# Kernel tuning notes

Measured on AMD Instinct MI355X. Metric: run time of the kernel, lower is better.

## Reference

```python
import jax, jax.numpy as jnp
import numpy as np
from jax.scipy.special import logsumexp

B, T, S, F = 16, 4096, 32, 64
LOG2PI = float(np.log(2.0 * np.pi))


def setup_inputs() -> dict:
    key = jax.random.key(0)
    k1, k2, k3, k4, k5 = jax.random.split(key, 5)
    x = jax.random.normal(k1, (B, T, F), dtype=jnp.float32)
    means = jax.random.normal(k2, (S, F), dtype=jnp.float32)
    # PSD full covariance per state: A A^T + I  (MultivariateNormal covariance_matrix)
    A = 0.1 * jax.random.normal(k3, (S, F, F), dtype=jnp.float32)
    covs = jnp.einsum('sfg,shg->sfh', A, A) + jnp.eye(F, dtype=jnp.float32)
    # Row-stochastic transition matrix and initial distribution, in log space.
    log_A = jax.nn.log_softmax(jax.random.normal(k4, (S, S), dtype=jnp.float32), axis=-1)
    log_pi = jax.nn.log_softmax(jax.random.normal(k5, (S,), dtype=jnp.float32))
    mask = jnp.ones((B, T), dtype=bool)
    return {'x': x, 'means': means, 'covs': covs, 'log_A': log_A, 'log_pi': log_pi, 'mask': mask}


def _emission_logprob(x, means, covs):
    # Multivariate Gaussian log pdf per (batch, time, state): logB[b,t,s]
    Fdim = x.shape[-1]
    P = jnp.linalg.inv(covs)                       # [S,F,F] precision
    logdet = jnp.linalg.slogdet(covs)[1]           # [S]
    diff = x[:, :, None, :] - means[None, None]    # [B,T,S,F]
    maha = jnp.einsum('btsf,sfg,btsg->bts', diff, P, diff)
    return -0.5 * (maha + Fdim * LOG2PI + logdet)


def _fb_single(logB, mask, log_A, log_pi):
    # Forward-backward DP for one sequence. logB: [T,S], mask: [T].
    neg_inf = jnp.array(-jnp.inf, logB.dtype)

    def fstep(a_prev, inp):
        lb, m = inp
        a = logsumexp(a_prev[:, None] + log_A, axis=0) + lb  # alpha[t,j]
        a = jnp.where(m, a, neg_inf)
        return a, a

    a0 = jnp.where(mask[0], log_pi + logB[0], neg_inf)
    _, alphas = jax.lax.scan(fstep, a0, (logB[1:], mask[1:]))
    alpha = jnp.concatenate([a0[None], alphas], axis=0)      # [T,S]

    def bstep(b_next, inp):
        lb_next, m_next = inp
        b = logsumexp(log_A + (lb_next + b_next)[None, :], axis=1)  # beta[t,j]
        b = jnp.where(m_next, b, b_next)  # freeze at 0 past the last valid frame
        return b, b

    bT = jnp.zeros(logB.shape[1], dtype=logB.dtype)
    _, betas = jax.lax.scan(bstep, bT, (logB[1:], mask[1:]), reverse=True)
    beta = jnp.concatenate([betas, bT[None]], axis=0)        # [T,S]
    beta = jnp.where(mask[:, None], beta, neg_inf)
    return alpha, beta


def reference(x, means, covs, log_A, log_pi, mask):
    logB = _emission_logprob(x, means, covs)                  # [B,T,S]
    alpha, beta = jax.vmap(_fb_single, in_axes=(0, 0, None, None))(logB, mask, log_A, log_pi)
    lengths = mask.sum(axis=-1)                               # [B]
    idx = jnp.broadcast_to((lengths - 1)[:, None, None], (alpha.shape[0], 1, alpha.shape[2]))
    alpha_last = jnp.take_along_axis(alpha, idx, axis=1)[:, 0, :]
    evidence = logsumexp(alpha_last, axis=-1)                 # [B] log p(x_{1:l})
    gamma = alpha + beta - evidence[:, None, None]            # log posterior state marginals
    return gamma
```

## Files before the change

kernel.cpp:

```cpp
#include <hip/hip_runtime.h>
#include <math.h>

#define Tt 4096
#define NB 16

#define CLN2PI 1.8378770664093453f

#define OFF_W    0
#define OFF_D    131072
#define OFF_CST  133120
#define OFF_EV   133152
#define OFF_LB   133184
#define OFF_BET  2230336

__device__ __forceinline__ float rdlane(float x, int l) {
  return __int_as_float(__builtin_amdgcn_readlane(__float_as_int(x), l));
}

typedef unsigned int u32x2 __attribute__((ext_vector_type(2)));
__device__ __forceinline__ void xhalf(float v, float& lo, float& hi) {
  u32x2 r = __builtin_amdgcn_permlane32_swap(__float_as_uint(v), __float_as_uint(v),
                                             false, false);
  lo = __uint_as_float(r.x);
  hi = __uint_as_float(r.y);
}

__global__ __launch_bounds__(64) void k_chol(const float* __restrict__ covs,
                                             const float* __restrict__ means,
                                             float* __restrict__ ws) {
  __shared__ float Am[64][65];
  __shared__ float Wl[64][65];
  int s = blockIdx.x, j = threadIdx.x;
  for (int r = 0; r < 64; ++r) {
    Am[r][j] = covs[((size_t)s * 64 + r) * 64 + j];
    Wl[r][j] = 0.f;
  }
  __syncthreads();
  for (int k = 0; k < 64; ++k) {
    float diag = sqrtf(Am[k][k]);
    float col = (j > k) ? Am[j][k] / diag : 0.f;
    __syncthreads();
    if (j == k) Am[k][k] = diag;
    if (j > k)  Am[j][k] = col;
    __syncthreads();
    if (j > k) {
      for (int g = k + 1; g <= j; ++g) Am[j][g] -= col * Am[g][k];
    }
    __syncthreads();
  }
  {
    int c = j;
    Wl[c][c] = 1.0f / Am[c][c];
    for (int f = c + 1; f < 64; ++f) {
      float ssum = 0.f;
      for (int g = c; g < f; ++g) ssum += Am[f][g] * Wl[g][c];
      Wl[f][c] = -ssum / Am[f][f];
    }
  }
  __syncthreads();
  for (int r = 0; r < 64; ++r)
    ws[OFF_W + ((size_t)s * 64 + r) * 64 + j] = Wl[r][j];
  {
    float acc = 0.f;
    for (int g = 0; g < 64; ++g) acc += Wl[j][g] * means[s * 64 + g];
    ws[OFF_D + s * 64 + j] = acc;
  }
  if (j == 0) {
    float logdet = 0.f;
    for (int k = 0; k < 64; ++k) logdet += __logf(Am[k][k]);
    logdet *= 2.0f;
    ws[OFF_CST + s] = 64.0f * CLN2PI + logdet;
  }
}

__global__ __launch_bounds__(64) void k_emis(const float* __restrict__ x,
                                             const float* __restrict__ wsr,
                                             float* __restrict__ lb) {
  const float* W = wsr + OFF_W;
  const float* D = wsr + OFF_D;
  const float* C = wsr + OFF_CST;
  int bx = blockIdx.x;
  int sgrp = bx & 3;
  int pt = (bx >> 2) * 64 + threadIdx.x;
  const float* xr = x + (size_t)pt * 64;
  float xv[64];
#pragma unroll
  for (int c = 0; c < 16; ++c) {
    float4 q = ((const float4*)xr)[c];
    xv[4 * c + 0] = q.x; xv[4 * c + 1] = q.y;
    xv[4 * c + 2] = q.z; xv[4 * c + 3] = q.w;
  }
#pragma unroll 1
  for (int si = 0; si < 8; ++si) {
    int s = sgrp * 8 + si;
    const float* Ws = W + (size_t)s * 4096;
    const float* Ds = D + s * 64;
    float maha = 0.f;
#pragma unroll
    for (int f = 0; f < 64; ++f) {
      float z = -Ds[f];
#pragma unroll
      for (int ch = 0; ch < 4; ++ch) {
        if (ch <= (f >> 4)) {
#pragma unroll
          for (int gg = 0; gg < 16; ++gg) {
            int g = ch * 16 + gg;
            z = fmaf(Ws[f * 64 + g], xv[g], z);
          }
        }
      }
      maha = fmaf(z, z, maha);
    }
    lb[(size_t)pt * 32 + s] = -0.5f * (maha + C[s]);
  }
}

__device__ __forceinline__ float npsum32(const float* z) {
  float r[8];
#pragma unroll
  for (int k = 0; k < 8; ++k)
    r[k] = ((z[k] + z[k + 8]) + z[k + 16]) + z[k + 24];
  return ((r[0] + r[1]) + (r[2] + r[3])) + ((r[4] + r[5]) + (r[6] + r[7]));
}
__device__ __forceinline__ float max32(const float* z) {
  float t16[16];
#pragma unroll
  for (int k = 0; k < 16; ++k) t16[k] = fmaxf(z[k], z[k + 16]);
  float t8[8];
#pragma unroll
  for (int k = 0; k < 8; ++k) t8[k] = fmaxf(t16[k], t16[k + 8]);
  float t4[4];
#pragma unroll
  for (int k = 0; k < 4; ++k) t4[k] = fmaxf(t8[k], t8[k + 4]);
  float t2a = fmaxf(t4[0], t4[2]), t2b = fmaxf(t4[1], t4[3]);
  return fmaxf(t2a, t2b);
}
__device__ __forceinline__ float max16(const float* z) {
  float t8[8];
#pragma unroll
  for (int k = 0; k < 8; ++k) t8[k] = fmaxf(z[k], z[k + 8]);
  float t4[4];
#pragma unroll
  for (int k = 0; k < 4; ++k) t4[k] = fmaxf(t8[k], t8[k + 4]);
  return fmaxf(fmaxf(t4[0], t4[2]), fmaxf(t4[1], t4[3]));
}
__device__ __forceinline__ float sum16(const float* e) {
  float t8[8];
#pragma unroll
  for (int k = 0; k < 8; ++k) t8[k] = e[k] + e[k + 8];
  float t4[4];
#pragma unroll
  for (int k = 0; k < 4; ++k) t4[k] = t8[k] + t8[k + 4];
  return (t4[0] + t4[2]) + (t4[1] + t4[3]);
}

__global__ __launch_bounds__(64, 1) __attribute__((amdgpu_waves_per_eu(1)))
void k_fb(const float* __restrict__ logA,
          const float* __restrict__ logpi,
          float* __restrict__ ws,
          float* __restrict__ out) {
  const float* lbg = ws + OFF_LB;
  float* bet = ws + OFF_BET;
  float* ev  = ws + OFF_EV;
  int chain = blockIdx.x;
  int b   = chain & 15;
  int dir = chain >> 4;
  int lane = threadIdx.x;
  int j = lane & 31;
  int h = lane >> 5;
  int i0 = h << 4;
  const float* lb = lbg + (size_t)b * Tt * 32;

  if (dir == 0) {
    float acol[16];
#pragma unroll
    for (int k = 0; k < 16; ++k) {
      acol[k] = logA[(i0 + k) * 32 + j];
      asm volatile("" : "+v"(acol[k]));
    }
    float* ao = out + (size_t)b * Tt * 32;
    float a = logpi[j] + lb[j];
    ao[j] = a;
    float bA = lb[32 + j];
    float bB = lb[64 + j];
    float bC = lb[96 + j];
#pragma unroll 1
    for (int t = 1; t < Tt; ++t) {
      float bcur = bA; bA = bB; bB = bC;
      if (t + 3 < Tt) bC = lb[(size_t)(t + 3) * 32 + j];
      float sa[32];
#pragma unroll
      for (int i = 0; i < 32; ++i) sa[i] = rdlane(a, i);
      float z[16];
      if (h == 0) {
#pragma unroll
        for (int k = 0; k < 16; ++k) z[k] = sa[k] + acol[k];
      } else {
#pragma unroll
        for (int k = 0; k < 16; ++k) z[k] = sa[16 + k] + acol[k];
      }
      float mh = max16(z);
      float mlo, mhi;
      xhalf(mh, mlo, mhi);
      float m = fmaxf(mlo, mhi);
      float e[16];
#pragma unroll
      for (int k = 0; k < 16; ++k) e[k] = __expf(z[k] - m);
      float sh = sum16(e);
      float slo, shi;
      xhalf(sh, slo, shi);
      float S = slo + shi;
      a = (__logf(S) + m) + bcur;
      ao[(size_t)t * 32 + j] = a;
    }
    float z[32];
#pragma unroll
    for (int i = 0; i < 32; ++i) z[i] = rdlane(a, i);
    float m = max32(z);
#pragma unroll
    for (int i = 0; i < 32; ++i) z[i] = __expf(z[i] - m);
    float S = npsum32(z);
    if (lane == 0) ev[b] = __logf(S) + m;
  } else {
    float arow[16];
#pragma unroll
    for (int k = 0; k < 16; ++k) {
      arow[k] = logA[j * 32 + i0 + k];
      asm volatile("" : "+v"(arow[k]));
    }
    float* bo = bet + (size_t)b * Tt * 32;
    bo[(size_t)(Tt - 1) * 32 + j] = 0.f;
    float y = lb[(size_t)(Tt - 1) * 32 + j] + 0.f;
    float bA = lb[(size_t)(Tt - 2) * 32 + j];
    float bB = lb[(size_t)(Tt - 3) * 32 + j];
    float bC = lb[(size_t)(Tt - 4) * 32 + j];
#pragma unroll 1
    for (int t = Tt - 2; t >= 0; --t) {
      float bcur = bA; bA = bB; bB = bC;
      if (t >= 3) bC = lb[(size_t)(t - 3) * 32 + j];
      float sy[32];
#pragma unroll
      for (int i = 0; i < 32; ++i) sy[i] = rdlane(y, i);
      float z[16];
      if (h == 0) {
#pragma unroll
        for (int k = 0; k < 16; ++k) z[k] = arow[k] + sy[k];
      } else {
#pragma unroll
        for (int k = 0; k < 16; ++k) z[k] = arow[k] + sy[16 + k];
      }
      float mh = max16(z);
      float mlo, mhi;
      xhalf(mh, mlo, mhi);
      float m = fmaxf(mlo, mhi);
      float e[16];
#pragma unroll
      for (int k = 0; k < 16; ++k) e[k] = __expf(z[k] - m);
      float sh = sum16(e);
      float slo, shi;
      xhalf(sh, slo, shi);
      float S = slo + shi;
      float bv = __logf(S) + m;
      bo[(size_t)t * 32 + j] = bv;
      y = bcur + bv;
    }
  }
}

__global__ void k_gamma(const float* __restrict__ ws, float* __restrict__ out) {
  size_t idx = (size_t)blockIdx.x * blockDim.x + threadIdx.x;
  if (idx >= (size_t)NB * Tt * 32) return;
  int b = (int)(idx >> 17);
  float a  = out[idx];
  float bb = ws[OFF_BET + idx];
  float e  = ws[OFF_EV + b];
  out[idx] = (a + bb) - e;
}

extern "C" void kernel_launch(void* const* d_in, const int* in_sizes, int n_in,
                              void* d_out, int out_size, void* d_ws, size_t ws_size,
                              hipStream_t stream) {
  const float* x     = (const float*)d_in[0];
  const float* means = (const float*)d_in[1];
  const float* covs  = (const float*)d_in[2];
  const float* logA  = (const float*)d_in[3];
  const float* logpi = (const float*)d_in[4];
  float* ws  = (float*)d_ws;
  float* out = (float*)d_out;

  k_chol<<<dim3(32), dim3(64), 0, stream>>>(covs, means, ws);
  k_emis<<<dim3(4096), dim3(64), 0, stream>>>(x, ws, ws + OFF_LB);
  k_fb<<<dim3(32), dim3(64), 0, stream>>>(logA, logpi, ws, out);
  k_gamma<<<dim3(8192), dim3(256), 0, stream>>>(ws, out);
}
```

Measured before the change: 2.221 ms.

## Interleave forward and backward recursions in one wave per sequence

Instead of running the forward and backward chains in separate single-wave blocks (32 blocks), each block now runs both chains for one sequence in the same loop iteration (16 blocks). The two chains are independent, so interleaving them gives the scheduler instruction-level parallelism to hide the long dependent readlane/exp/log latency of each step. The cost is higher register pressure and twice the per-iteration work in one wave, which may not beat running the chains as separate waves on separate CUs.

```diff
diff --git a/kernel.cpp b/kernel.cpp
--- a/kernel.cpp
+++ b/kernel.cpp
@@ -162,109 +162,107 @@
   const float* lbg = ws + OFF_LB;
   float* bet = ws + OFF_BET;
   float* ev  = ws + OFF_EV;
-  int chain = blockIdx.x;
-  int b   = chain & 15;
-  int dir = chain >> 4;
+  int b   = blockIdx.x;
   int lane = threadIdx.x;
   int j = lane & 31;
   int h = lane >> 5;
   int i0 = h << 4;
   const float* lb = lbg + (size_t)b * Tt * 32;
-
-  if (dir == 0) {
-    float acol[16];
-#pragma unroll
-    for (int k = 0; k < 16; ++k) {
-      acol[k] = logA[(i0 + k) * 32 + j];
-      asm volatile("" : "+v"(acol[k]));
-    }
-    float* ao = out + (size_t)b * Tt * 32;
-    float a = logpi[j] + lb[j];
-    ao[j] = a;
-    float bA = lb[32 + j];
-    float bB = lb[64 + j];
-    float bC = lb[96 + j];
+  float* ao = out + (size_t)b * Tt * 32;
+  float* bo = bet + (size_t)b * Tt * 32;
+
+  float acol[16];
+  float arow[16];
+#pragma unroll
+  for (int k = 0; k < 16; ++k) {
+    acol[k] = logA[(i0 + k) * 32 + j];
+    asm volatile("" : "+v"(acol[k]));
+  }
+#pragma unroll
+  for (int k = 0; k < 16; ++k) {
+    arow[k] = logA[j * 32 + i0 + k];
+    asm volatile("" : "+v"(arow[k]));
+  }
+
+  float aF = logpi[j] + lb[j];
+  ao[j] = aF;
+  float fA = lb[32 + j];
+  float fB = lb[64 + j];
+  float fC = lb[96 + j];
+  bo[(size_t)(Tt - 1) * 32 + j] = 0.f;
+  float yB = lb[(size_t)(Tt - 1) * 32 + j] + 0.f;
+  float gA = lb[(size_t)(Tt - 2) * 32 + j];
+  float gB = lb[(size_t)(Tt - 3) * 32 + j];
+  float gC = lb[(size_t)(Tt - 4) * 32 + j];
+
 #pragma unroll 1
-    for (int t = 1; t < Tt; ++t) {
-      float bcur = bA; bA = bB; bB = bC;
-      if (t + 3 < Tt) bC = lb[(size_t)(t + 3) * 32 + j];
-      float sa[32];
-#pragma unroll
-      for (int i = 0; i < 32; ++i) sa[i] = rdlane(a, i);
-      float z[16];
-      if (h == 0) {
-#pragma unroll
-        for (int k = 0; k < 16; ++k) z[k] = sa[k] + acol[k];
-      } else {
-#pragma unroll
-        for (int k = 0; k < 16; ++k) z[k] = sa[16 + k] + acol[k];
-      }
-      float mh = max16(z);
-      float mlo, mhi;
-      xhalf(mh, mlo, mhi);
-      float m = fmaxf(mlo, mhi);
-      float e[16];
-#pragma unroll
-      for (int k = 0; k < 16; ++k) e[k] = __expf(z[k] - m);
-      float sh = sum16(e);
-      float slo, shi;
-      xhalf(sh, slo, shi);
-      float S = slo + shi;
-      a = (__logf(S) + m) + bcur;
-      ao[(size_t)t * 32 + j] = a;
-    }
-    float z[32];
-#pragma unroll
-    for (int i = 0; i < 32; ++i) z[i] = rdlane(a, i);
-    float m = max32(z);
-#pragma unroll
-    for (int i = 0; i < 32; ++i) z[i] = __expf(z[i] - m);
-    float S = npsum32(z);
-    if (lane == 0) ev[b] = __logf(S) + m;
-  } else {
-    float arow[16];
-#pragma unroll
-    for (int k = 0; k < 16; ++k) {
-      arow[k] = logA[j * 32 + i0 + k];
-      asm volatile("" : "+v"(arow[k]));
-    }
-    float* bo = bet + (size_t)b * Tt * 32;
-    bo[(size_t)(Tt - 1) * 32 + j] = 0.f;
-    float y = lb[(size_t)(Tt - 1) * 32 + j] + 0.f;
-    float bA = lb[(size_t)(Tt - 2) * 32 + j];
-    float bB = lb[(size_t)(Tt - 3) * 32 + j];
-    float bC = lb[(size_t)(Tt - 4) * 32 + j];
-#pragma unroll 1
-    for (int t = Tt - 2; t >= 0; --t) {
-      float bcur = bA; bA = bB; bB = bC;
-      if (t >= 3) bC = lb[(size_t)(t - 3) * 32 + j];
-      float sy[32];
-#pragma unroll
-      for (int i = 0; i < 32; ++i) sy[i] = rdlane(y, i);
-      float z[16];
-      if (h == 0) {
-#pragma unroll
-        for (int k = 0; k < 16; ++k) z[k] = arow[k] + sy[k];
-      } else {
-#pragma unroll
-        for (int k = 0; k < 16; ++k) z[k] = arow[k] + sy[16 + k];
-      }
-      float mh = max16(z);
-      float mlo, mhi;
-      xhalf(mh, mlo, mhi);
-      float m = fmaxf(mlo, mhi);
-      float e[16];
-#pragma unroll
-      for (int k = 0; k < 16; ++k) e[k] = __expf(z[k] - m);
-      float sh = sum16(e);
-      float slo, shi;
-      xhalf(sh, slo, shi);
-      float S = slo + shi;
-      float bv = __logf(S) + m;
-      bo[(size_t)t * 32 + j] = bv;
-      y = bcur + bv;
-    }
-  }
+  for (int n = 1; n < Tt; ++n) {
+    int tb = Tt - 1 - n;
+    float bf = fA; fA = fB; fB = fC;
+    if (n + 3 < Tt) fC = lb[(size_t)(n + 3) * 32 + j];
+    float bg = gA; gA = gB; gB = gC;
+    if (tb >= 3) gC = lb[(size_t)(tb - 3) * 32 + j];
+
+    float saF[32];
+#pragma unroll
+    for (int i = 0; i < 32; ++i) saF[i] = rdlane(aF, i);
+    float zF[16];
+    if (h == 0) {
+#pragma unroll
+      for (int k = 0; k < 16; ++k) zF[k] = saF[k] + acol[k];
+    } else {
+#pragma unroll
+      for (int k = 0; k < 16; ++k) zF[k] = saF[16 + k] + acol[k];
+    }
+    float mhF = max16(zF);
+    float mloF, mhiF;
+    xhalf(mhF, mloF, mhiF);
+    float mF = fmaxf(mloF, mhiF);
+    float eF[16];
+#pragma unroll
+    for (int k = 0; k < 16; ++k) eF[k] = __expf(zF[k] - mF);
+    float shF = sum16(eF);
+    float sloF, shiF;
+    xhalf(shF, sloF, shiF);
+    float SF = sloF + shiF;
+    aF = (__logf(SF) + mF) + bf;
+    ao[(size_t)n * 32 + j] = aF;
+
+    float syB[32];
+#pragma unroll
+    for (int i = 0; i < 32; ++i) syB[i] = rdlane(yB, i);
+    float zB[16];
+    if (h == 0) {
+#pragma unroll
+      for (int k = 0; k < 16; ++k) zB[k] = arow[k] + syB[k];
+    } else {
+#pragma unroll
+      for (int k = 0; k < 16; ++k) zB[k] = arow[k] + syB[16 + k];
+    }
+    float mhB = max16(zB);
+    float mloB, mhiB;
+    xhalf(mhB, mloB, mhiB);
+    float mB = fmaxf(mloB, mhiB);
+    float eB[16];
+#pragma unroll
+    for (int k = 0; k < 16; ++k) eB[k] = __expf(zB[k] - mB);
+    float shB = sum16(eB);
+    float sloB, shiB;
+    xhalf(shB, sloB, shiB);
+    float SB = sloB + shiB;
+    float bv = __logf(SB) + mB;
+    bo[(size_t)tb * 32 + j] = bv;
+    yB = bg + bv;
+  }
+
+  float z[32];
+#pragma unroll
+  for (int i = 0; i < 32; ++i) z[i] = rdlane(aF, i);
+  float m = max32(z);
+#pragma unroll
+  for (int i = 0; i < 32; ++i) z[i] = __expf(z[i] - m);
+  float S = npsum32(z);
+  if (lane == 0) ev[b] = __logf(S) + m;
 }
 
 __global__ void k_gamma(const float* __restrict__ ws, float* __restrict__ out) {
@@ -290,6 +288,6 @@
 
   k_chol<<<dim3(32), dim3(64), 0, stream>>>(covs, means, ws);
   k_emis<<<dim3(4096), dim3(64), 0, stream>>>(x, ws, ws + OFF_LB);
-  k_fb<<<dim3(32), dim3(64), 0, stream>>>(logA, logpi, ws, out);
+  k_fb<<<dim3(16), dim3(64), 0, stream>>>(logA, logpi, ws, out);
   k_gamma<<<dim3(8192), dim3(256), 0, stream>>>(ws, out);
 }
```

After: 3.602 ms. 62.2% more time.
